# Performance work log

Hardware: AMD Instinct MI355X
Metric: run time of the kernel (lower is better)

## Reference

```python
import jax, jax.numpy as jnp
import numpy as np

D_MODEL, D_INNER, D_CONV, D_STATE, DT_RANK = 1024, 2048, 4, 16, 64
ALPHA, CHUNK = 0.1, 64


def setup_inputs() -> dict:
    key = jax.random.key(0)
    ks = jax.random.split(key, 10)
    B, T = 2, 2048
    s = lambda k, shape, scale: jax.random.normal(k, shape, jnp.float32) * scale
    return {
        "x": s(ks[0], (B, T, D_MODEL), 1.0),
        "norm1_w": jnp.ones((D_MODEL,), jnp.float32),
        "norm2_w": jnp.ones((D_MODEL,), jnp.float32),
        "in_proj_w": s(ks[1], (2 * D_INNER, D_MODEL), 0.02),
        "in_proj_b": jnp.zeros((2 * D_INNER,), jnp.float32),
        "conv_w": s(ks[2], (D_INNER, 1, D_CONV), 0.1),
        "conv_b": jnp.zeros((D_INNER,), jnp.float32),
        "x_proj_w": s(ks[3], (DT_RANK + 2 * D_STATE, D_INNER), 0.02),
        "dt_proj_w": s(ks[4], (D_INNER, DT_RANK), 0.02),
        "dt_proj_b": s(ks[5], (D_INNER,), 0.02),
        "A_log": jnp.log(jnp.broadcast_to(jnp.arange(1, D_STATE + 1, dtype=jnp.float32), (D_INNER, D_STATE))) + 0.0,
        "D_ssm": jnp.ones((D_INNER,), jnp.float32),
        "out_proj_w": s(ks[6], (D_MODEL, D_INNER), 0.02),
        "out_proj_b": jnp.zeros((D_MODEL,), jnp.float32),
        "proj_write_w": s(ks[7], (D_MODEL, D_MODEL), 0.02),
        "proj_read_w": s(ks[8], (D_MODEL, D_MODEL), 0.02),
        "decay": jnp.float32(4.6),
    }


def rmsnorm(x, w, eps=1e-5):
    return x * jax.lax.rsqrt(jnp.mean(x * x, axis=-1, keepdims=True) + eps) * w


def mamba_block(x, in_w, in_b, conv_w, conv_b, xp_w, dt_w, dt_b, A_log, D_ssm, out_w, out_b):
    # canonical (mamba-minimal) selective-SSM block
    B, T, _ = x.shape
    xz = x @ in_w.T + in_b                      # (B,T,2*d_inner)
    xm, res = jnp.split(xz, 2, axis=-1)
    # causal depthwise conv over time
    xc = jax.lax.conv_general_dilated(
        xm.transpose(0, 2, 1), conv_w, (1,), [(D_CONV - 1, 0)],
        dimension_numbers=("NCH", "OIH", "NCH"), feature_group_count=D_INNER)
    xm = jax.nn.silu(xc.transpose(0, 2, 1) + conv_b)
    x_dbl = xm @ xp_w.T                         # (B,T,dt_rank+2*d_state)
    delta = jax.nn.softplus(x_dbl[..., :DT_RANK] @ dt_w.T + dt_b)
    Bm = x_dbl[..., DT_RANK:DT_RANK + D_STATE]
    Cm = x_dbl[..., DT_RANK + D_STATE:]
    A = -jnp.exp(A_log)                          # (d_inner, d_state)

    def step(h, ins):
        d_t, B_t, C_t, u_t = ins                 # (B,di),(B,ds),(B,ds),(B,di)
        dA = jnp.exp(d_t[:, :, None] * A)
        h = h * dA + (d_t * u_t)[:, :, None] * B_t[:, None, :]
        y = jnp.einsum("bds,bs->bd", h, C_t)
        return h, y

    h0 = jnp.zeros((B, D_INNER, D_STATE), x.dtype)
    _, ys = jax.lax.scan(step, h0, (delta.transpose(1, 0, 2), Bm.transpose(1, 0, 2),
                                    Cm.transpose(1, 0, 2), xm.transpose(1, 0, 2)))
    y = ys.transpose(1, 0, 2) + xm * D_ssm
    y = y * jax.nn.silu(res)
    return y @ out_w.T + out_b


def memory_attend(out, w_write, w_read, decay):
    # chunked Hebbian write/read (RetNet-style chunked linear attention)
    B, T, D = out.shape
    C = CHUNK
    gamma = jax.nn.sigmoid(decay)
    log_gamma = jnp.log(gamma)
    v = out @ w_write.T
    wk = jnp.pad(out[:, :-1], ((0, 0), (1, 0), (0, 0)))
    rk = out
    n = T // C
    p = jnp.arange(C)
    diffs = jnp.clip(p[:, None] - 1 - p[None, :], 0, None).astype(out.dtype)
    causal = (p[:, None] > p[None, :]).astype(out.dtype)
    M = jnp.exp(diffs * log_gamma) * causal      # (C,C) intra-chunk decay mask
    g_in = gamma ** p                            # (C,)
    g_w = gamma ** (C - 1 - p)                   # (C,)

    chunked = lambda a: a.reshape(B, n, C, D).transpose(1, 0, 2, 3)  # (n,B,C,D)

    def step(W, ins):
        rk_c, wk_c, v_c = ins                    # each (B,C,D)
        inter = jnp.einsum("bde,bce->bcd", W, rk_c) * g_in[None, :, None]
        S = jnp.einsum("bcd,bkd->bck", rk_c, wk_c)
        intra = jnp.einsum("bck,bkd->bcd", S * M, v_c)
        W_new = (gamma ** C) * W + jnp.einsum("bcd,bce->bde", v_c * g_w[None, :, None], wk_c)
        return W_new, inter + intra

    W0 = jnp.zeros((B, D, D), out.dtype)
    _, reads = jax.lax.scan(step, W0, (chunked(rk), chunked(wk), chunked(v)))
    reads = reads.transpose(1, 0, 2, 3).reshape(B, T, D)
    return out + ALPHA * (reads @ w_read.T)


def reference(x, norm1_w, norm2_w, in_proj_w, in_proj_b, conv_w, conv_b, x_proj_w,
              dt_proj_w, dt_proj_b, A_log, D_ssm, out_proj_w, out_proj_b,
              proj_write_w, proj_read_w, decay):
    mb = lambda h: mamba_block(h, in_proj_w, in_proj_b, conv_w, conv_b, x_proj_w,
                               dt_proj_w, dt_proj_b, A_log, D_ssm, out_proj_w, out_proj_b)
    out1 = mb(rmsnorm(x, norm1_w))
    x1 = x + out1
    out2 = mb(rmsnorm(x1, norm2_w))   # tied weights: same params as mamba1
    out2 = memory_attend(out2, proj_write_w, proj_read_w, decay)
    return x1 + out2
```

## Files before the change

kernel.cpp:

```cpp
#include <hip/hip_runtime.h>
#include <hip/hip_bf16.h>
#include <math.h>

typedef __hip_bfloat16 bf16;
typedef __attribute__((ext_vector_type(4))) float f32x4;
typedef __attribute__((ext_vector_type(8))) short bf16x8;
typedef __attribute__((ext_vector_type(8))) unsigned short u16x8;

static __device__ __forceinline__ float b2f(bf16 v) { return __bfloat162float(v); }
static __device__ __forceinline__ float us2f(unsigned short u) {
  union { unsigned short s; bf16 h; } c; c.s = u; return __bfloat162float(c.h);
}
static __device__ __forceinline__ void  stv(float* p, float v) { *p = v; }
static __device__ __forceinline__ void  stv(bf16* p, float v) { *p = __float2bfloat16(v); }
static __device__ __forceinline__ float ldin(const void* p, size_t i, int f) {
  return f ? ((const float*)p)[i] : b2f(((const bf16*)p)[i]);
}
static __device__ __forceinline__ unsigned short f2b(float x) {
  bf16 h = __float2bfloat16(x);
  return *reinterpret_cast<unsigned short*>(&h);
}

static __device__ __forceinline__ void gl16(const unsigned short* g,
                                            void* ldsbase, int byteoff) {
  __builtin_amdgcn_global_load_lds(
      (const __attribute__((address_space(1))) unsigned int*)g,
      (__attribute__((address_space(3))) unsigned int*)((char*)ldsbase + byteoff),
      16, 0, 0);
}

constexpr int B_  = 2;
constexpr int T_  = 2048;
constexpr int DM  = 1024;
constexpr int DI  = 2048;
constexpr int DS  = 16;
constexpr int DTR = 64;
constexpr int ROWS = B_ * T_;
constexpr int SL  = 32;
constexpr int NSC = T_ / SL;
constexpr int KSP = 4;

__global__ void detect_k(const void* __restrict__ decay, int* __restrict__ flag) {
  flag[0] = (((const unsigned short*)decay)[0] == 0x4093) ? 0 : 1;
  flag[1] = 0;
}

__global__ void sentinel_k(void* __restrict__ out, float val, int n,
                           const int* __restrict__ df) {
  int f = *df;
  int i = blockIdx.x * 256 + threadIdx.x;
  if (i < n) {
    if (f) ((float*)out)[i] = val;
    else   ((bf16*)out)[i] = __float2bfloat16(val);
  }
}

__global__ void cvt1_k(const void* __restrict__ src, bf16* __restrict__ dst, int n,
                       const int* __restrict__ df) {
  int f = *df;
  int i = blockIdx.x * 256 + threadIdx.x;
  if (i < n) stv(&dst[i], ldin(src, i, f));
}

__global__ void rmsnorm_k(const void* __restrict__ xin, const void* __restrict__ w,
                          bf16* __restrict__ out, const int* __restrict__ df,
                          int xin_raw) {
  int f = *df;
  int fx = xin_raw ? f : 0;
  int row = blockIdx.x;
  int tid = threadIdx.x;
  float ss = 0.f;
  for (int d = tid; d < DM; d += 256) {
    float v = ldin(xin, (size_t)row * DM + d, fx);
    ss += v * v;
  }
  for (int o = 32; o > 0; o >>= 1) ss += __shfl_down(ss, o, 64);
  __shared__ float sred[4];
  int lane = tid & 63, wid = tid >> 6;
  if (lane == 0) sred[wid] = ss;
  __syncthreads();
  if (tid == 0) {
    float t = sred[0] + sred[1] + sred[2] + sred[3];
    sred[0] = 1.f / sqrtf(t / DM + 1e-5f);
  }
  __syncthreads();
  float rs = sred[0];
  for (int d = tid; d < DM; d += 256) {
    float v = ldin(xin, (size_t)row * DM + d, fx);
    stv(&out[(size_t)row * DM + d], v * rs * ldin(w, d, f));
  }
}

__global__ void transpose_k(const bf16* __restrict__ src, bf16* __restrict__ dst) {
  __shared__ unsigned short tile[64][65];
  int b = blockIdx.z;
  int t0 = blockIdx.x * 64, d0 = blockIdx.y * 64;
  int tid = threadIdx.x;
  int lt = tid & 63, lq = tid >> 6;
  const unsigned short* sp = (const unsigned short*)src;
  unsigned short* dp = (unsigned short*)dst;
#pragma unroll
  for (int i = 0; i < 16; i++) {
    int r = lq * 16 + i;
    tile[r][lt] = sp[((size_t)b * T_ + t0 + r) * DM + d0 + lt];
  }
  __syncthreads();
#pragma unroll
  for (int i = 0; i < 16; i++) {
    int r = lq * 16 + i;
    dp[((size_t)b * DM + d0 + r) * T_ + t0 + lt] = tile[lt][r];
  }
}

template <int MODE, int ACT, int MROWS>
__global__ void mgemm_k(const bf16* __restrict__ A, size_t sAz, int lda,
                        const void* __restrict__ B, size_t sBz, int ldb,
                        const void* __restrict__ bias,
                        bf16* __restrict__ C, size_t sCz, int ldc,
                        int M, int N, int K,
                        const void* __restrict__ dec, const int* __restrict__ df) {
  constexpr int FR = MROWS / 32;
  int by = (MODE == 2) ? ((int)gridDim.y - 1 - (int)blockIdx.y) : (int)blockIdx.y;
  int m0 = by * MROWS, n0 = blockIdx.x * 128;
  if (MODE == 1 && n0 > m0 + MROWS - 1) return;
  int f = *df;
  int bz = blockIdx.z;
  const bf16* Ab = A + (size_t)bz * sAz;
  const unsigned short* Bb16 =
      (const unsigned short*)B + (size_t)bz * sBz;
  bf16* Cb = C + (size_t)bz * sCz;
  int kmax = (MODE == 2) ? (m0 + MROWS) : K;
  __shared__ alignas(16) unsigned short As[MROWS][32];
  __shared__ alignas(16) unsigned short Bs[128][32];
  int tid = threadIdx.x;
  int wave = tid >> 6, lane = tid & 63, quad = lane >> 4, l15 = lane & 15;
  int wr = (wave >> 1) * (MROWS / 2), wc = (wave & 1) * 64;
  f32x4 acc[FR][4] = {};
  int lrow = lane >> 2;
  int lh   = (lane & 3) * 8;
  const unsigned short* Aus = (const unsigned short*)Ab;
  for (int k0 = 0; k0 < kmax; k0 += 32) {
    if (MROWS == 128) {
#pragma unroll
      for (int q = 0; q < 2; q++) {
        int seg = wave * 2 + q;
        int rowa = seg * 16 + lrow;
        gl16(Aus + (size_t)(m0 + rowa) * lda + k0 + lh, &As[0][0], seg * 1024);
      }
    } else {
      int rowa = wave * 16 + lrow;
      gl16(Aus + (size_t)(m0 + rowa) * lda + k0 + lh, &As[0][0], wave * 1024);
    }
    if (MODE == 0 && f) {
      int r = tid >> 1, h = (tid & 1) * 16;
      const float* bp = (const float*)B + (size_t)(n0 + r) * ldb + k0 + h;
      float4 x0 = *(const float4*)bp,       x1 = *(const float4*)(bp + 4);
      float4 x2 = *(const float4*)(bp + 8), x3 = *(const float4*)(bp + 12);
      union { unsigned short s[8]; uint4 v; } p0, p1;
      p0.s[0]=f2b(x0.x); p0.s[1]=f2b(x0.y); p0.s[2]=f2b(x0.z); p0.s[3]=f2b(x0.w);
      p0.s[4]=f2b(x1.x); p0.s[5]=f2b(x1.y); p0.s[6]=f2b(x1.z); p0.s[7]=f2b(x1.w);
      p1.s[0]=f2b(x2.x); p1.s[1]=f2b(x2.y); p1.s[2]=f2b(x2.z); p1.s[3]=f2b(x2.w);
      p1.s[4]=f2b(x3.x); p1.s[5]=f2b(x3.y); p1.s[6]=f2b(x3.z); p1.s[7]=f2b(x3.w);
      *(uint4*)&Bs[r][h]     = p0.v;
      *(uint4*)&Bs[r][h + 8] = p1.v;
    } else {
#pragma unroll
      for (int q = 0; q < 2; q++) {
        int seg = wave * 2 + q;
        int rowb = seg * 16 + lrow;
        gl16(Bb16 + (size_t)(n0 + rowb) * ldb + k0 + lh, &Bs[0][0], seg * 1024);
      }
    }
    __syncthreads();
    bf16x8 af[FR], bfv[4];
#pragma unroll
    for (int i = 0; i < FR; i++)
      af[i] = *(const bf16x8*)&As[wr + 16 * i + l15][quad * 8];
#pragma unroll
    for (int j = 0; j < 4; j++)
      bfv[j] = *(const bf16x8*)&Bs[wc + 16 * j + l15][quad * 8];
#pragma unroll
    for (int i = 0; i < FR; i++)
#pragma unroll
      for (int j = 0; j < 4; j++)
        acc[i][j] = __builtin_amdgcn_mfma_f32_16x16x32_bf16(af[i], bfv[j],
                                                            acc[i][j], 0, 0, 0);
    __syncthreads();
  }
  float lg = 0.f;
  if (MODE == 1) {
    float g = 1.f / (1.f + __expf(-ldin(dec, 0, f)));
    lg = __logf(g);
  }
#pragma unroll
  for (int i = 0; i < FR; i++) {
#pragma unroll
    for (int rr = 0; rr < 4; rr++) {
      int row = m0 + wr + 16 * i + quad * 4 + rr;
      if (MODE == 1 && n0 == 0 && wc == 0 && l15 == 0)
        Cb[(size_t)row * ldc] = __float2bfloat16(0.f);
#pragma unroll
      for (int j = 0; j < 4; j++) {
        int col = n0 + wc + 16 * j + l15;
        float v = acc[i][j][rr];
        if (MODE == 0) {
          if (bias) v += ldin(bias, col, f);
          if (ACT == 1) v = (v > 20.f) ? v : log1pf(__expf(v));
          Cb[(size_t)row * ldc + col] = __float2bfloat16(v);
        } else if (MODE == 1) {
          int colp = col + 1;
          int d_ = row - colp;
          v = (d_ > 0) ? v * __expf(lg * (float)(d_ - 1)) : 0.f;
          if (colp < N)
            Cb[(size_t)row * ldc + colp] = __float2bfloat16(v);
        } else {
          Cb[(size_t)row * ldc + col] = __float2bfloat16(v);
        }
      }
    }
  }
}

__global__ void conv_silu_k(const bf16* __restrict__ xz, const void* __restrict__ cw,
                            const void* __restrict__ cb, bf16* __restrict__ xm,
                            const int* __restrict__ df) {
  int f = *df;
  int i = blockIdx.x * 256 + threadIdx.x;
  int d = i & (DI - 1);
  int t = (i >> 11) & (T_ - 1);
  int b = i >> 22;
  const bf16* base = xz + (size_t)b * T_ * 2 * DI + d;
  float s = ldin(cb, d, f);
#pragma unroll
  for (int k = 0; k < 4; k++) {
    int tt = t - 3 + k;
    if (tt >= 0) s += ldin(cw, d * 4 + k, f) * b2f(base[(size_t)tt * 2 * DI]);
  }
  stv(&xm[i], s / (1.f + __expf(-s)));
}

__global__ void xproj_k(const bf16* __restrict__ xm, const void* __restrict__ xpw,
                        bf16* __restrict__ parts, const int* __restrict__ df) {
  int f = *df;
  int m0 = blockIdx.x * 128;
  int z = blockIdx.y;
  int kbase = z * (DI / KSP);
  __shared__ alignas(16) unsigned short As[128][32];
  __shared__ alignas(16) unsigned short Bs[96][32];
  int tid = threadIdx.x;
  int wave = tid >> 6, lane = tid & 63, quad = lane >> 4, l15 = lane & 15;
  int wr = wave * 32;
  f32x4 acc[2][6] = {};
  int lrow = lane >> 2;
  int lh   = (lane & 3) * 8;
  const unsigned short* Aus = (const unsigned short*)xm;
  const unsigned short* Bus = (const unsigned short*)xpw;
  for (int k0 = 0; k0 < DI / KSP; k0 += 32) {
#pragma unroll
    for (int q = 0; q < 2; q++) {
      int seg = wave * 2 + q;
      int rowa = seg * 16 + lrow;
      gl16(Aus + (size_t)(m0 + rowa) * DI + kbase + k0 + lh, &As[0][0], seg * 1024);
    }
    if (f) {
      if (tid < 192) {
        int r2 = tid >> 1, h2 = (tid & 1) * 16;
        const float* bp = (const float*)xpw + (size_t)r2 * DI + kbase + k0 + h2;
        float4 x0 = *(const float4*)bp,       x1 = *(const float4*)(bp + 4);
        float4 x2 = *(const float4*)(bp + 8), x3 = *(const float4*)(bp + 12);
        union { unsigned short s[8]; uint4 v; } p0, p1;
        p0.s[0]=f2b(x0.x); p0.s[1]=f2b(x0.y); p0.s[2]=f2b(x0.z); p0.s[3]=f2b(x0.w);
        p0.s[4]=f2b(x1.x); p0.s[5]=f2b(x1.y); p0.s[6]=f2b(x1.z); p0.s[7]=f2b(x1.w);
        p1.s[0]=f2b(x2.x); p1.s[1]=f2b(x2.y); p1.s[2]=f2b(x2.z); p1.s[3]=f2b(x2.w);
        p1.s[4]=f2b(x3.x); p1.s[5]=f2b(x3.y); p1.s[6]=f2b(x3.z); p1.s[7]=f2b(x3.w);
        *(uint4*)&Bs[r2][h2]     = p0.v;
        *(uint4*)&Bs[r2][h2 + 8] = p1.v;
      }
    } else if (wave < 3) {
#pragma unroll
      for (int q = 0; q < 2; q++) {
        int seg = wave * 2 + q;
        int rowb = seg * 16 + lrow;
        gl16(Bus + (size_t)rowb * DI + kbase + k0 + lh, &Bs[0][0], seg * 1024);
      }
    }
    __syncthreads();
    bf16x8 af[2], bfv[6];
#pragma unroll
    for (int i = 0; i < 2; i++)
      af[i] = *(const bf16x8*)&As[wr + 16 * i + l15][quad * 8];
#pragma unroll
    for (int j = 0; j < 6; j++)
      bfv[j] = *(const bf16x8*)&Bs[16 * j + l15][quad * 8];
#pragma unroll
    for (int i = 0; i < 2; i++)
#pragma unroll
      for (int j = 0; j < 6; j++)
        acc[i][j] = __builtin_amdgcn_mfma_f32_16x16x32_bf16(af[i], bfv[j],
                                                            acc[i][j], 0, 0, 0);
    __syncthreads();
  }
  bf16* out = parts + (size_t)z * ROWS * 96;
#pragma unroll
  for (int i = 0; i < 2; i++)
#pragma unroll
    for (int rr = 0; rr < 4; rr++) {
      int row = m0 + wr + 16 * i + quad * 4 + rr;
#pragma unroll
      for (int j = 0; j < 6; j++) {
        int col = 16 * j + l15;
        out[(size_t)row * 96 + col] = __float2bfloat16(acc[i][j][rr]);
      }
    }
}

__global__ void reduce_xdbl_k(const bf16* __restrict__ parts, bf16* __restrict__ xdbl) {
  int i = blockIdx.x * 256 + threadIdx.x;
  if (i >= ROWS * 96) return;
  float s = 0.f;
#pragma unroll
  for (int z = 0; z < KSP; z++) s += b2f(parts[(size_t)z * ROWS * 96 + i]);
  stv(&xdbl[i], s);
}

__global__ void scan_p1_k(const bf16* __restrict__ delta, const bf16* __restrict__ xm,
                          const bf16* __restrict__ xdbl,
                          const void* __restrict__ alog,
                          bf16* __restrict__ F, float* __restrict__ S,
                          const int* __restrict__ df) {
  int f = *df;
  int idx = blockIdx.x * 256 + threadIdx.x;
  int d = idx & (DI - 1);
  int c = (idx >> 11) & (NSC - 1);
  int b = idx >> 17;
  float A[DS], hh[DS];
  bool fastA = true;
#pragma unroll
  for (int s = 0; s < DS; s++) {
    A[s] = -__expf(ldin(alog, d * DS + s, f));
    fastA = fastA && (fabsf(A[s] + (float)(s + 1)) < 1e-3f);
    hh[s] = 0.f;
  }
  int cs = c * SL;
  float ssum = 0.f;
  if (fastA) {
    for (int t = cs; t < cs + SL; t++) {
      size_t r = (size_t)b * T_ + t;
      float dlt = b2f(delta[r * DI + d]);
      float u = b2f(xm[r * DI + d]);
      ssum += dlt;
      float du = dlt * u;
      float q = __expf(-dlt);
      u16x8 t0 = *(const u16x8*)(xdbl + r * 96 + 64);
      u16x8 t1 = *(const u16x8*)(xdbl + r * 96 + 72);
      float e = 1.f;
#pragma unroll
      for (int s = 0; s < 8; s++) {
        e *= q; hh[s] = hh[s] * e + du * us2f(t0[s]);
      }
#pragma unroll
      for (int s = 0; s < 8; s++) {
        e *= q; hh[8 + s] = hh[8 + s] * e + du * us2f(t1[s]);
      }
    }
  } else {
    for (int t = cs; t < cs + SL; t++) {
      size_t r = (size_t)b * T_ + t;
      float dlt = b2f(delta[r * DI + d]);
      float u = b2f(xm[r * DI + d]);
      ssum += dlt;
      float du = dlt * u;
      u16x8 t0 = *(const u16x8*)(xdbl + r * 96 + 64);
      u16x8 t1 = *(const u16x8*)(xdbl + r * 96 + 72);
#pragma unroll
      for (int s = 0; s < 8; s++) {
        hh[s]     = hh[s]     * __expf(dlt * A[s])     + du * us2f(t0[s]);
        hh[8 + s] = hh[8 + s] * __expf(dlt * A[8 + s]) + du * us2f(t1[s]);
      }
    }
  }
#pragma unroll
  for (int s = 0; s < DS; s++) stv(&F[(size_t)idx * 16 + s], hh[s]);
  S[idx] = ssum;
}

__global__ void scan_p2_k(bf16* __restrict__ F, const float* __restrict__ S,
                          const void* __restrict__ alog, const int* __restrict__ df) {
  int f = *df;
  int idx = blockIdx.x * 256 + threadIdx.x;
  int s = idx & 15;
  int d = (idx >> 4) & (DI - 1);
  int b = idx >> 15;
  float As_ = -__expf(ldin(alog, d * DS + s, f));
  float H = 0.f;
  for (int c = 0; c < NSC; c++) {
    size_t base = (size_t)(b * NSC + c) * DI + d;
    float tmp = b2f(F[base * 16 + s]);
    stv(&F[base * 16 + s], H);
    H = __expf(As_ * S[base]) * H + tmp;
  }
}

__global__ void scan_p3_k(bf16* __restrict__ delta, const bf16* __restrict__ xm,
                          const bf16* __restrict__ xz, const bf16* __restrict__ xdbl,
                          const void* __restrict__ alog, const void* __restrict__ dssm,
                          const bf16* __restrict__ F, const int* __restrict__ df) {
  int f = *df;
  int idx = blockIdx.x * 256 + threadIdx.x;
  int d = idx & (DI - 1);
  int c = (idx >> 11) & (NSC - 1);
  int b = idx >> 17;
  float A[DS], hh[DS];
  bool fastA = true;
#pragma unroll
  for (int s = 0; s < DS; s++) {
    A[s] = -__expf(ldin(alog, d * DS + s, f));
    fastA = fastA && (fabsf(A[s] + (float)(s + 1)) < 1e-3f);
    hh[s] = b2f(F[(size_t)idx * 16 + s]);
  }
  float Dv = ldin(dssm, d, f);
  int cs = c * SL;
  if (fastA) {
    for (int t = cs; t < cs + SL; t++) {
      size_t r = (size_t)b * T_ + t;
      float dlt = b2f(delta[r * DI + d]);
      float u = b2f(xm[r * DI + d]);
      float du = dlt * u;
      float q = __expf(-dlt);
      u16x8 t0 = *(const u16x8*)(xdbl + r * 96 + 64);
      u16x8 t1 = *(const u16x8*)(xdbl + r * 96 + 72);
      u16x8 t2 = *(const u16x8*)(xdbl + r * 96 + 80);
      u16x8 t3 = *(const u16x8*)(xdbl + r * 96 + 88);
      float y = 0.f;
      float e = 1.f;
#pragma unroll
      for (int s = 0; s < 8; s++) {
        e *= q;
        hh[s] = hh[s] * e + du * us2f(t0[s]);
        y += hh[s] * us2f(t2[s]);
      }
#pragma unroll
      for (int s = 0; s < 8; s++) {
        e *= q;
        hh[8 + s] = hh[8 + s] * e + du * us2f(t1[s]);
        y += hh[8 + s] * us2f(t3[s]);
      }
      float res = b2f(xz[r * 2 * DI + DI + d]);
      y += u * Dv;
      y *= res / (1.f + __expf(-res));
      stv(&delta[r * DI + d], y);
    }
  } else {
    for (int t = cs; t < cs + SL; t++) {
      size_t r = (size_t)b * T_ + t;
      float dlt = b2f(delta[r * DI + d]);
      float u = b2f(xm[r * DI + d]);
      float du = dlt * u;
      u16x8 t0 = *(const u16x8*)(xdbl + r * 96 + 64);
      u16x8 t1 = *(const u16x8*)(xdbl + r * 96 + 72);
      u16x8 t2 = *(const u16x8*)(xdbl + r * 96 + 80);
      u16x8 t3 = *(const u16x8*)(xdbl + r * 96 + 88);
      float y = 0.f;
#pragma unroll
      for (int s = 0; s < 8; s++) {
        hh[s]     = hh[s]     * __expf(dlt * A[s])     + du * us2f(t0[s]);
        hh[8 + s] = hh[8 + s] * __expf(dlt * A[8 + s]) + du * us2f(t1[s]);
        y += hh[s] * us2f(t2[s]) + hh[8 + s] * us2f(t3[s]);
      }
      float res = b2f(xz[r * 2 * DI + DI + d]);
      y += u * Dv;
      y *= res / (1.f + __expf(-res));
      stv(&delta[r * DI + d], y);
    }
  }
}

__global__ void add_x1_k(const void* __restrict__ x, const bf16* __restrict__ o1,
                         bf16* __restrict__ x1, const int* __restrict__ df) {
  int f = *df;
  int i = blockIdx.x * 256 + threadIdx.x;
  if (i < ROWS * DM) stv(&x1[i], ldin(x, i, f) + b2f(o1[i]));
}

__global__ void final_k(const bf16* __restrict__ x1, const bf16* __restrict__ out2,
                        const bf16* __restrict__ rproj, void* __restrict__ out,
                        const int* __restrict__ df) {
  int f = *df;
  int i = blockIdx.x * 256 + threadIdx.x;
  if (i < ROWS * DM) {
    float v = b2f(x1[i]) + b2f(out2[i]) + 0.1f * b2f(rproj[i]);
    if (f) ((float*)out)[i] = v;
    else   stv(&((bf16*)out)[i], v);
  }
}

extern "C" void kernel_launch(void* const* d_in, const int* in_sizes, int n_in,
                              void* d_out, int out_size, void* d_ws, size_t ws_size,
                              hipStream_t stream) {
  (void)in_sizes; (void)n_in;
  const void* x    = d_in[0];
  const void* n1w  = d_in[1];
  const void* n2w  = d_in[2];
  const void* ipw  = d_in[3];
  const void* ipb  = d_in[4];
  const void* cw   = d_in[5];
  const void* cb   = d_in[6];
  const void* xpw  = d_in[7];
  const void* dtw  = d_in[8];
  const void* dtb  = d_in[9];
  const void* alog = d_in[10];
  const void* dssm = d_in[11];
  const void* opw  = d_in[12];
  const void* opb  = d_in[13];
  const void* pww  = d_in[14];
  const void* prw  = d_in[15];
  const void* dec  = d_in[16];

  char* base = (char*)d_ws;
  bf16*  xz    = (bf16*) (base + 0);
  bf16*  v     = (bf16*) (base + 0);
  bf16*  reads = (bf16*) (base + 8388608);
  bf16*  P     = (bf16*) (base + 16777216);
  bf16*  delta = (bf16*) (base + 33554432);
  bf16*  hnorm = delta;
  bf16*  rproj = (bf16*) (base + 33554432);
  bf16*  vt    = (bf16*) (base + 41943040);
  bf16*  xm    = (bf16*) (base + 50331648);
  bf16*  xdbl  = (bf16*) (base + 67108864);
  bf16*  parts = (bf16*) (base + 67895296);
  float* S     = (float*)(base + 67895296);
  bf16*  bout  = (bf16*) (base + 71041024);
  bf16*  F     = (bf16*) (base + 71041024);
  bf16*  x1    = (bf16*) (base + 79429632);
  int*   dflag = (int*)  (base + 87818240);
  bf16*  wbuf  = (bf16*) (base + 87818256);
  constexpr size_t WS_MIN = 87818248;
  constexpr int O_IPW = 0;
  constexpr int O_OPW = 4194304;
  constexpr int O_PWW = 6291456;
  constexpr int O_PRW = 7340032;
  constexpr int O_XPW = 8388608;
  constexpr int O_DTW = 8585216;
  constexpr int O_IPB = 8716288;
  constexpr int O_OPB = 8720384;
  constexpr int O_DTB = 8721408;
  constexpr int W_TOT = 8723456;
  constexpr size_t WS_BIG = 87818256 + (size_t)W_TOT * 2;

  detect_k<<<1, 1, 0, stream>>>(dec, dflag);
  if (ws_size < WS_MIN) {
    sentinel_k<<<(out_size + 255) / 256, 256, 0, stream>>>(
        d_out, (float)(ws_size >> 20), out_size, dflag);
    return;
  }

  const void *g_ipw = ipw, *g_ipb = ipb, *g_xpw = xpw, *g_dtw = dtw,
             *g_dtb = dtb, *g_opw = opw, *g_opb = opb, *g_pww = pww, *g_prw = prw;
  const int* wf = dflag;
  if (ws_size >= WS_BIG) {
    auto cvt = [&](const void* src, int off, int n) {
      cvt1_k<<<(n + 255) / 256, 256, 0, stream>>>(src, wbuf + off, n, dflag);
    };
    cvt(ipw, O_IPW, 4194304); cvt(opw, O_OPW, 2097152);
    cvt(pww, O_PWW, 1048576); cvt(prw, O_PRW, 1048576);
    cvt(xpw, O_XPW, 196608);  cvt(dtw, O_DTW, 131072);
    cvt(ipb, O_IPB, 4096);    cvt(opb, O_OPB, 1024);   cvt(dtb, O_DTB, 2048);
    g_ipw = wbuf + O_IPW; g_opw = wbuf + O_OPW; g_pww = wbuf + O_PWW;
    g_prw = wbuf + O_PRW; g_xpw = wbuf + O_XPW; g_dtw = wbuf + O_DTW;
    g_ipb = wbuf + O_IPB; g_opb = wbuf + O_OPB; g_dtb = wbuf + O_DTB;
    wf = dflag + 1;
  }

  auto mamba = [&](const void* xin, int xin_raw, const void* nw, bf16* outb) {
    rmsnorm_k<<<ROWS, 256, 0, stream>>>(xin, nw, hnorm, dflag, xin_raw);
    mgemm_k<0, 0, 128><<<dim3(32, 32, 1), 256, 0, stream>>>(
        hnorm, 0, DM, g_ipw, 0, DM, g_ipb, xz, 0, 2 * DI, ROWS, 2 * DI, DM, dec, wf);
    conv_silu_k<<<(ROWS * DI) / 256, 256, 0, stream>>>(xz, cw, cb, xm, dflag);
    xproj_k<<<dim3(32, KSP), 256, 0, stream>>>(xm, g_xpw, parts, wf);
    reduce_xdbl_k<<<(ROWS * 96) / 256, 256, 0, stream>>>(parts, xdbl);
    mgemm_k<0, 1, 128><<<dim3(16, 32, 1), 256, 0, stream>>>(
        xdbl, 0, 96, g_dtw, 0, DTR, g_dtb, delta, 0, DI, ROWS, DI, DTR, dec, wf);
    scan_p1_k<<<B_ * NSC * DI / 256, 256, 0, stream>>>(delta, xm, xdbl, alog, F, S, dflag);
    scan_p2_k<<<B_ * DI * 16 / 256, 256, 0, stream>>>(F, S, alog, dflag);
    scan_p3_k<<<B_ * NSC * DI / 256, 256, 0, stream>>>(delta, xm, xz, xdbl, alog, dssm, F, dflag);
    mgemm_k<0, 0, 64><<<dim3(8, 64, 1), 256, 0, stream>>>(
        delta, 0, DI, g_opw, 0, DI, g_opb, outb, 0, DM, ROWS, DM, DI, dec, wf);
  };

  mamba(x, 1, n1w, bout);
  add_x1_k<<<(ROWS * DM) / 256, 256, 0, stream>>>(x, bout, x1, dflag);
  mamba(x1, 0, n2w, bout);

  mgemm_k<0, 0, 64><<<dim3(8, 64, 1), 256, 0, stream>>>(
      bout, 0, DM, g_pww, 0, DM, nullptr, v, 0, DM, ROWS, DM, DM, dec, wf);
  transpose_k<<<dim3(T_ / 64, DM / 64, B_), 256, 0, stream>>>(v, vt);
  mgemm_k<1, 0, 64><<<dim3(16, 32, B_), 256, 0, stream>>>(
      bout, (size_t)T_ * DM, DM, bout, (size_t)T_ * DM, DM, nullptr,
      P, (size_t)T_ * T_, T_, T_, T_, DM, dec, dflag);
  mgemm_k<2, 0, 64><<<dim3(8, 32, B_), 256, 0, stream>>>(
      P, (size_t)T_ * T_, T_, vt, (size_t)DM * T_, T_, nullptr,
      reads, (size_t)T_ * DM, DM, T_, DM, T_, dec, dflag);
  mgemm_k<0, 0, 64><<<dim3(8, 64, 1), 256, 0, stream>>>(
      reads, 0, DM, g_prw, 0, DM, nullptr, rproj, 0, DM, ROWS, DM, DM, dec, wf);
  final_k<<<(ROWS * DM) / 256, 256, 0, stream>>>(x1, bout, rproj, d_out, dflag);
}
```

Before: 862.7 us.

## Double-buffer LDS tiles in MFMA GEMM and x_proj kernels

Converts the shared-memory A/B tiles in the generic GEMM kernel and the x_proj kernel into two buffers. The next K-slice is loaded while MFMAs run on the current one, which drops one barrier per iteration and lets global-load latency overlap compute. This doubles LDS use per block, which can lower occupancy. The fp32-to-bf16 convert path for B still stalls on its global loads before the compute step.

```diff
diff --git a/kernel.cpp b/kernel.cpp
--- a/kernel.cpp
+++ b/kernel.cpp
@@ -130,8 +130,8 @@
       (const unsigned short*)B + (size_t)bz * sBz;
   bf16* Cb = C + (size_t)bz * sCz;
   int kmax = (MODE == 2) ? (m0 + MROWS) : K;
-  __shared__ alignas(16) unsigned short As[MROWS][32];
-  __shared__ alignas(16) unsigned short Bs[128][32];
+  __shared__ alignas(16) unsigned short As[2][MROWS][32];
+  __shared__ alignas(16) unsigned short Bs[2][128][32];
   int tid = threadIdx.x;
   int wave = tid >> 6, lane = tid & 63, quad = lane >> 4, l15 = lane & 15;
   int wr = (wave >> 1) * (MROWS / 2), wc = (wave & 1) * 64;
@@ -139,17 +139,20 @@
   int lrow = lane >> 2;
   int lh   = (lane & 3) * 8;
   const unsigned short* Aus = (const unsigned short*)Ab;
-  for (int k0 = 0; k0 < kmax; k0 += 32) {
+
+  auto stage = [&](int buf, int k0) {
     if (MROWS == 128) {
 #pragma unroll
       for (int q = 0; q < 2; q++) {
         int seg = wave * 2 + q;
         int rowa = seg * 16 + lrow;
-        gl16(Aus + (size_t)(m0 + rowa) * lda + k0 + lh, &As[0][0], seg * 1024);
+        gl16(Aus + (size_t)(m0 + rowa) * lda + k0 + lh, &As[buf][0][0],
+             seg * 1024);
       }
     } else {
       int rowa = wave * 16 + lrow;
-      gl16(Aus + (size_t)(m0 + rowa) * lda + k0 + lh, &As[0][0], wave * 1024);
+      gl16(Aus + (size_t)(m0 + rowa) * lda + k0 + lh, &As[buf][0][0],
+           wave * 1024);
     }
     if (MODE == 0 && f) {
       int r = tid >> 1, h = (tid & 1) * 16;
@@ -161,32 +164,47 @@
       p0.s[4]=f2b(x1.x); p0.s[5]=f2b(x1.y); p0.s[6]=f2b(x1.z); p0.s[7]=f2b(x1.w);
       p1.s[0]=f2b(x2.x); p1.s[1]=f2b(x2.y); p1.s[2]=f2b(x2.z); p1.s[3]=f2b(x2.w);
       p1.s[4]=f2b(x3.x); p1.s[5]=f2b(x3.y); p1.s[6]=f2b(x3.z); p1.s[7]=f2b(x3.w);
-      *(uint4*)&Bs[r][h]     = p0.v;
-      *(uint4*)&Bs[r][h + 8] = p1.v;
+      *(uint4*)&Bs[buf][r][h]     = p0.v;
+      *(uint4*)&Bs[buf][r][h + 8] = p1.v;
     } else {
 #pragma unroll
       for (int q = 0; q < 2; q++) {
         int seg = wave * 2 + q;
         int rowb = seg * 16 + lrow;
-        gl16(Bb16 + (size_t)(n0 + rowb) * ldb + k0 + lh, &Bs[0][0], seg * 1024);
-      }
-    }
-    __syncthreads();
+        gl16(Bb16 + (size_t)(n0 + rowb) * ldb + k0 + lh, &Bs[buf][0][0],
+             seg * 1024);
+      }
+    }
+  };
+
+  auto compute = [&](int buf) {
     bf16x8 af[FR], bfv[4];
 #pragma unroll
     for (int i = 0; i < FR; i++)
-      af[i] = *(const bf16x8*)&As[wr + 16 * i + l15][quad * 8];
+      af[i] = *(const bf16x8*)&As[buf][wr + 16 * i + l15][quad * 8];
 #pragma unroll
     for (int j = 0; j < 4; j++)
-      bfv[j] = *(const bf16x8*)&Bs[wc + 16 * j + l15][quad * 8];
+      bfv[j] = *(const bf16x8*)&Bs[buf][wc + 16 * j + l15][quad * 8];
 #pragma unroll
     for (int i = 0; i < FR; i++)
 #pragma unroll
       for (int j = 0; j < 4; j++)
         acc[i][j] = __builtin_amdgcn_mfma_f32_16x16x32_bf16(af[i], bfv[j],
                                                             acc[i][j], 0, 0, 0);
+  };
+
+  int nt = kmax >> 5;
+  stage(0, 0);
+  __syncthreads();
+  int cur = 0;
+  for (int t = 0; t < nt - 1; ++t) {
+    stage(cur ^ 1, (t + 1) * 32);
+    compute(cur);
     __syncthreads();
-  }
+    cur ^= 1;
+  }
+  compute(cur);
+
   float lg = 0.f;
   if (MODE == 1) {
     float g = 1.f / (1.f + __expf(-ldin(dec, 0, f)));
@@ -245,8 +263,8 @@
   int m0 = blockIdx.x * 128;
   int z = blockIdx.y;
   int kbase = z * (DI / KSP);
-  __shared__ alignas(16) unsigned short As[128][32];
-  __shared__ alignas(16) unsigned short Bs[96][32];
+  __shared__ alignas(16) unsigned short As[2][128][32];
+  __shared__ alignas(16) unsigned short Bs[2][96][32];
   int tid = threadIdx.x;
   int wave = tid >> 6, lane = tid & 63, quad = lane >> 4, l15 = lane & 15;
   int wr = wave * 32;
@@ -255,12 +273,14 @@
   int lh   = (lane & 3) * 8;
   const unsigned short* Aus = (const unsigned short*)xm;
   const unsigned short* Bus = (const unsigned short*)xpw;
-  for (int k0 = 0; k0 < DI / KSP; k0 += 32) {
+
+  auto stage = [&](int buf, int k0) {
 #pragma unroll
     for (int q = 0; q < 2; q++) {
       int seg = wave * 2 + q;
       int rowa = seg * 16 + lrow;
-      gl16(Aus + (size_t)(m0 + rowa) * DI + kbase + k0 + lh, &As[0][0], seg * 1024);
+      gl16(Aus + (size_t)(m0 + rowa) * DI + kbase + k0 + lh, &As[buf][0][0],
+           seg * 1024);
     }
     if (f) {
       if (tid < 192) {
@@ -273,33 +293,48 @@
         p0.s[4]=f2b(x1.x); p0.s[5]=f2b(x1.y); p0.s[6]=f2b(x1.z); p0.s[7]=f2b(x1.w);
         p1.s[0]=f2b(x2.x); p1.s[1]=f2b(x2.y); p1.s[2]=f2b(x2.z); p1.s[3]=f2b(x2.w);
         p1.s[4]=f2b(x3.x); p1.s[5]=f2b(x3.y); p1.s[6]=f2b(x3.z); p1.s[7]=f2b(x3.w);
-        *(uint4*)&Bs[r2][h2]     = p0.v;
-        *(uint4*)&Bs[r2][h2 + 8] = p1.v;
+        *(uint4*)&Bs[buf][r2][h2]     = p0.v;
+        *(uint4*)&Bs[buf][r2][h2 + 8] = p1.v;
       }
     } else if (wave < 3) {
 #pragma unroll
       for (int q = 0; q < 2; q++) {
         int seg = wave * 2 + q;
         int rowb = seg * 16 + lrow;
-        gl16(Bus + (size_t)rowb * DI + kbase + k0 + lh, &Bs[0][0], seg * 1024);
-      }
-    }
-    __syncthreads();
+        gl16(Bus + (size_t)rowb * DI + kbase + k0 + lh, &Bs[buf][0][0],
+             seg * 1024);
+      }
+    }
+  };
+
+  auto compute = [&](int buf) {
     bf16x8 af[2], bfv[6];
 #pragma unroll
     for (int i = 0; i < 2; i++)
-      af[i] = *(const bf16x8*)&As[wr + 16 * i + l15][quad * 8];
+      af[i] = *(const bf16x8*)&As[buf][wr + 16 * i + l15][quad * 8];
 #pragma unroll
     for (int j = 0; j < 6; j++)
-      bfv[j] = *(const bf16x8*)&Bs[16 * j + l15][quad * 8];
+      bfv[j] = *(const bf16x8*)&Bs[buf][16 * j + l15][quad * 8];
 #pragma unroll
     for (int i = 0; i < 2; i++)
 #pragma unroll
       for (int j = 0; j < 6; j++)
         acc[i][j] = __builtin_amdgcn_mfma_f32_16x16x32_bf16(af[i], bfv[j],
                                                             acc[i][j], 0, 0, 0);
+  };
+
+  constexpr int NT = (DI / KSP) / 32;
+  stage(0, 0);
+  __syncthreads();
+  int cur = 0;
+  for (int t = 0; t < NT - 1; ++t) {
+    stage(cur ^ 1, (t + 1) * 32);
+    compute(cur);
     __syncthreads();
-  }
+    cur ^= 1;
+  }
+  compute(cur);
+
   bf16* out = parts + (size_t)z * ROWS * 96;
 #pragma unroll
   for (int i = 0; i < 2; i++)
```

Measured after the change: 862.2 us. About the same (-0.0%).
